# Performance work log

Measured on AMD Instinct MI355X. Metric: run time of the kernel, lower is better.

The kernel has to match this reference:

```python
import jax, jax.numpy as jnp
import numpy as np

B, S, D, F = 8, 2048, 1024, 3072
EPS = 1e-6


def _rmsnorm(x, w):
    rms = jax.lax.rsqrt(jnp.mean(x * x, axis=-1, keepdims=True) + EPS)
    return x * rms * w


def _scan_causal(x_scan, a):
    # h_t = a_t * h_{t-1} + x_t, over time axis. x_scan, a: [B,S,D]
    def step(h, inp):
        xs, at = inp
        h = at * h + xs
        return h, h
    xs_t = jnp.swapaxes(x_scan, 0, 1)  # [S,B,D]
    a_t = jnp.swapaxes(a, 0, 1)
    h0 = jnp.zeros(x_scan.shape[::2], dtype=x_scan.dtype)  # [B,D]
    _, out = jax.lax.scan(step, h0, (xs_t, a_t))
    return jnp.swapaxes(out, 0, 1)  # [B,S,D]


def setup_inputs() -> dict:
    key = jax.random.key(0)
    ks = jax.random.split(key, 12)
    sd = 1.0 / np.sqrt(D)
    sf = 1.0 / np.sqrt(F)
    return {
        "x": jax.random.normal(ks[0], (B, S, D), dtype=jnp.float32),
        "rms_mix_w": jnp.ones((D,), jnp.float32),
        "rms_ffn_w": jnp.ones((D,), jnp.float32),
        "Wg": jax.random.uniform(ks[1], (D, D), jnp.float32, -sd, sd),
        "bg": jax.random.uniform(ks[2], (D,), jnp.float32, -sd, sd),
        "Wv": jax.random.uniform(ks[3], (D, D), jnp.float32, -sd, sd),
        "bv": jax.random.uniform(ks[4], (D,), jnp.float32, -sd, sd),
        "Wd": jax.random.uniform(ks[5], (D, D), jnp.float32, -sd, sd),
        "bd": jnp.full((D,), 1.0, jnp.float32),  # decay_bias_init = 1.0
        "W_gate": jax.random.uniform(ks[6], (F, D), jnp.float32, -sd, sd),
        "W_up": jax.random.uniform(ks[7], (F, D), jnp.float32, -sd, sd),
        "W_out": jax.random.uniform(ks[8], (D, F), jnp.float32, -sf, sf),
    }


def reference(x, rms_mix_w, rms_ffn_w, Wg, bg, Wv, bv, Wd, bd, W_gate, W_up, W_out):
    # --- MinGRU mixer with pre-RMSNorm and residual ---
    xn = _rmsnorm(x, rms_mix_w)
    g = jnp.einsum("bsd,ed->bse", xn, Wg) + bg
    v = jnp.einsum("bsd,ed->bse", xn, Wv) + bv
    d = jnp.einsum("bsd,ed->bse", xn, Wd) + bd
    x_scan = jax.nn.sigmoid(g) * jnp.tanh(v)
    a = 0.001 + 0.998 * jax.nn.sigmoid(d)
    x = x + _scan_causal(x_scan, a)
    # --- SwiGLU FFN with pre-RMSNorm and residual ---
    xn = _rmsnorm(x, rms_ffn_w)
    gate = jax.nn.silu(jnp.einsum("bsd,fd->bsf", xn, W_gate))
    up = jnp.einsum("bsd,fd->bsf", xn, W_up)
    x = x + jnp.einsum("bsf,df->bsd", gate * up, W_out)
    return x
```

## Files before the change

### kernel.cpp

```cpp
#include <hip/hip_runtime.h>
#include <cstdint>
#include <cstddef>

typedef unsigned short u16;
typedef __attribute__((ext_vector_type(4))) float f32x4;
typedef __attribute__((ext_vector_type(8))) short s16x8;

#define BB 8
#define SS 2048
#define DD 1024
#define FF 3072
#define MM (BB*SS)
#define NCH 64
#define LCH (SS/NCH)

__device__ __forceinline__ float bf2f(u16 u){ union{uint32_t i;float f;}v; v.i=((uint32_t)u)<<16; return v.f; }
__device__ __forceinline__ u16 f2bf(float f){ union{float f;uint32_t i;}v; v.f=f; uint32_t r=v.i+0x7FFFu+((v.i>>16)&1u); return (u16)(r>>16); }
__device__ __forceinline__ float sigm(float x){ return 1.f/(1.f+__expf(-x)); }
__device__ __forceinline__ float tanh_f(float x){ return 2.f*sigm(2.f*x)-1.f; }

__global__ void conv_all(const float* __restrict__ Wg, const float* __restrict__ Wv,
                         const float* __restrict__ Wd, const float* __restrict__ Wgate,
                         const float* __restrict__ Wup, const float* __restrict__ Wout,
                         const float* __restrict__ rfw,
                         u16* __restrict__ oGvd, u16* __restrict__ oGu, u16* __restrict__ oWo){
  const int blk = blockIdx.x;
  if (blk < 3072) {
    size_t i = ((size_t)blk*256 + threadIdx.x)*4;
    int row = (int)(i >> 10); int col = (int)(i & 1023);
    const float* src; int srow;
    if (row < 2048) { int grp = row >> 5, w = row & 31; src = (w < 16) ? Wg : Wv; srow = grp*16 + (w & 15); }
    else            { src = Wd; srow = row - 2048; }
    float4 v = *(const float4*)(src + (size_t)srow*1024 + col);
    ushort4 o; o.x=f2bf(v.x); o.y=f2bf(v.y); o.z=f2bf(v.z); o.w=f2bf(v.w);
    *(ushort4*)(oGvd + i) = o;
  } else if (blk < 9216) {
    size_t i = ((size_t)(blk-3072)*256 + threadIdx.x)*4;
    int row = (int)(i >> 10); int col = (int)(i & 1023);
    int group = row >> 5, w = row & 31;
    const float* src = (w < 16) ? Wgate : Wup;
    int srow = group*16 + (w & 15);
    float4 v = *(const float4*)(src + (size_t)srow*1024 + col);
    float4 s = *(const float4*)(rfw + col);
    ushort4 o; o.x=f2bf(v.x*s.x); o.y=f2bf(v.y*s.y); o.z=f2bf(v.z*s.z); o.w=f2bf(v.w*s.w);
    *(ushort4*)(oGu + i) = o;
  } else {
    size_t i = ((size_t)(blk-9216)*256 + threadIdx.x)*4;
    float4 v = *(const float4*)(Wout + i);
    ushort4 o; o.x=f2bf(v.x); o.y=f2bf(v.y); o.z=f2bf(v.z); o.w=f2bf(v.w);
    *(ushort4*)(oWo + i) = o;
  }
}

__global__ void rmsnorm_k(const float* __restrict__ x, const float* __restrict__ wgt,
                          u16* __restrict__ out){
  const int row = blockIdx.x, t = threadIdx.x;
  float4 v = ((const float4*)(x + (size_t)row*DD))[t];
  float ss = v.x*v.x + v.y*v.y + v.z*v.z + v.w*v.w;
  #pragma unroll
  for (int o = 32; o > 0; o >>= 1) ss += __shfl_down(ss, o, 64);
  __shared__ float sacc[4];
  if ((t & 63) == 0) sacc[t >> 6] = ss;
  __syncthreads();
  float tot = sacc[0] + sacc[1] + sacc[2] + sacc[3];
  float r = rsqrtf(tot * (1.f/(float)DD) + 1e-6f);
  float4 wv = ((const float4*)wgt)[t];
  ushort4 o; o.x=f2bf(v.x*r*wv.x); o.y=f2bf(v.y*r*wv.y); o.z=f2bf(v.z*r*wv.z); o.w=f2bf(v.w*r*wv.w);
  ((ushort4*)(out + (size_t)row*DD))[t] = o;
}

template<int EPI, int NTN>
__global__ __launch_bounds__(512) void gemm256(
    const u16* __restrict__ A, const u16* __restrict__ Bm, int K,
    const float* __restrict__ bg, const float* __restrict__ bv, const float* __restrict__ bd,
    const float* __restrict__ rinv,
    u16* __restrict__ o_xs, u16* __restrict__ o_a,
    u16* __restrict__ o_h, const u16* __restrict__ yres, float* __restrict__ o_out)
{
  __shared__ u16 lds[2*32768];
  const int tid = threadIdx.x, w = tid >> 6, l = tid & 63;
  const int wr = w >> 2, wc = w & 3;
  const int nwg = gridDim.x, bid = blockIdx.x;
  const int sw = (bid & 7) * (nwg >> 3) + (bid >> 3);
  const int tm = sw / NTN, tn = sw % NTN;

  const int srow  = w*8 + (l >> 3);
  const int sslot = (l & 7) ^ ((l >> 3) & 7);
  const u16* gA = A  + (size_t)(tm*256 + srow)*K + sslot*8;
  const u16* gB = Bm + (size_t)(tn*256 + srow)*K + sslot*8;

#define STAGE_HALF(dbuf, isB, h, tile) do { \
    const u16* gsrc_ = ((isB) ? gB : gA) + ((size_t)(h)*128)*K + (size_t)(tile)*64; \
    u16* ldst_ = &lds[(dbuf)*32768 + (isB)*16384 + (h)*8192 + w*512]; \
    __builtin_amdgcn_global_load_lds((const __attribute__((address_space(1))) void*)gsrc_, \
        (__attribute__((address_space(3))) void*)ldst_, 16, 0, 0); \
    __builtin_amdgcn_global_load_lds((const __attribute__((address_space(1))) void*)(gsrc_ + (size_t)64*K), \
        (__attribute__((address_space(3))) void*)(ldst_ + 4096), 16, 0, 0); \
  } while(0)

  const int aRow = wr*128 + (l & 15);
  const int bRow = wc*64  + (l & 15);
  const int sl0  = (((l >> 4) ^ (l & 7))) * 8;

#define LDA(cb, mi, ks) (*(const s16x8*)&lds[(cb)*32768 + (aRow + (mi)*16)*64 + (sl0 ^ ((ks)*32))])
#define LDB(cb, ni, ks) (*(const s16x8*)&lds[(cb)*32768 + 16384 + (bRow + (ni)*16)*64 + (sl0 ^ ((ks)*32))])

#define LOADB(cb) do { \
    bfr[0][0]=LDB(cb,0,0); bfr[0][1]=LDB(cb,0,1); \
    bfr[1][0]=LDB(cb,1,0); bfr[1][1]=LDB(cb,1,1); \
    bfr[2][0]=LDB(cb,2,0); bfr[2][1]=LDB(cb,2,1); \
    bfr[3][0]=LDB(cb,3,0); bfr[3][1]=LDB(cb,3,1); \
  } while(0)

#define PHASE(cb, mi0, STAGE_STMT, ...) do { \
    s16x8 a00 = LDA(cb, (mi0),   0), a01 = LDA(cb, (mi0),   1); \
    s16x8 a10 = LDA(cb, (mi0)+1, 0), a11 = LDA(cb, (mi0)+1, 1); \
    STAGE_STMT; \
    __builtin_amdgcn_s_barrier(); \
    asm volatile("s_waitcnt lgkmcnt(0)" ::: "memory"); \
    __builtin_amdgcn_s_setprio(1); \
    acc[(mi0)  ][0] = __builtin_amdgcn_mfma_f32_16x16x32_bf16(a00, bfr[0][0], acc[(mi0)  ][0],0,0,0); \
    acc[(mi0)  ][1] = __builtin_amdgcn_mfma_f32_16x16x32_bf16(a00, bfr[1][0], acc[(mi0)  ][1],0,0,0); \
    acc[(mi0)  ][2] = __builtin_amdgcn_mfma_f32_16x16x32_bf16(a00, bfr[2][0], acc[(mi0)  ][2],0,0,0); \
    acc[(mi0)  ][3] = __builtin_amdgcn_mfma_f32_16x16x32_bf16(a00, bfr[3][0], acc[(mi0)  ][3],0,0,0); \
    acc[(mi0)+1][0] = __builtin_amdgcn_mfma_f32_16x16x32_bf16(a10, bfr[0][0], acc[(mi0)+1][0],0,0,0); \
    acc[(mi0)+1][1] = __builtin_amdgcn_mfma_f32_16x16x32_bf16(a10, bfr[1][0], acc[(mi0)+1][1],0,0,0); \
    acc[(mi0)+1][2] = __builtin_amdgcn_mfma_f32_16x16x32_bf16(a10, bfr[2][0], acc[(mi0)+1][2],0,0,0); \
    acc[(mi0)+1][3] = __builtin_amdgcn_mfma_f32_16x16x32_bf16(a10, bfr[3][0], acc[(mi0)+1][3],0,0,0); \
    acc[(mi0)  ][0] = __builtin_amdgcn_mfma_f32_16x16x32_bf16(a01, bfr[0][1], acc[(mi0)  ][0],0,0,0); \
    acc[(mi0)  ][1] = __builtin_amdgcn_mfma_f32_16x16x32_bf16(a01, bfr[1][1], acc[(mi0)  ][1],0,0,0); \
    acc[(mi0)  ][2] = __builtin_amdgcn_mfma_f32_16x16x32_bf16(a01, bfr[2][1], acc[(mi0)  ][2],0,0,0); \
    acc[(mi0)  ][3] = __builtin_amdgcn_mfma_f32_16x16x32_bf16(a01, bfr[3][1], acc[(mi0)  ][3],0,0,0); \
    acc[(mi0)+1][0] = __builtin_amdgcn_mfma_f32_16x16x32_bf16(a11, bfr[0][1], acc[(mi0)+1][0],0,0,0); \
    acc[(mi0)+1][1] = __builtin_amdgcn_mfma_f32_16x16x32_bf16(a11, bfr[1][1], acc[(mi0)+1][1],0,0,0); \
    acc[(mi0)+1][2] = __builtin_amdgcn_mfma_f32_16x16x32_bf16(a11, bfr[2][1], acc[(mi0)+1][2],0,0,0); \
    acc[(mi0)+1][3] = __builtin_amdgcn_mfma_f32_16x16x32_bf16(a11, bfr[3][1], acc[(mi0)+1][3],0,0,0); \
    __builtin_amdgcn_s_setprio(0); \
    __VA_ARGS__; \
    __builtin_amdgcn_s_barrier(); \
  } while(0)

  f32x4 acc[8][4] = {};
  s16x8 bfr[4][2];
  const int nk = K >> 6;

  STAGE_HALF(0,0,0,0); STAGE_HALF(0,0,1,0);
  STAGE_HALF(0,1,0,0); STAGE_HALF(0,1,1,0);
  STAGE_HALF(1,1,0,1); STAGE_HALF(1,1,1,1);
  asm volatile("s_waitcnt vmcnt(4)" ::: "memory");
  __builtin_amdgcn_s_barrier();

  for (int it = 0, t = 0; it < (nk >> 1); ++it, t += 2) {
    const int tp1 = t + 1;
    int tp2 = t + 2; if (tp2 >= nk) tp2 -= nk;
    int tp3 = t + 3; if (tp3 >= nk) tp3 -= nk;
    LOADB(0);
    PHASE(0, 0, STAGE_HALF(1,0,0,tp1), );
    PHASE(0, 2, STAGE_HALF(1,0,1,tp1), );
    PHASE(0, 4, STAGE_HALF(0,1,0,tp2), );
    PHASE(0, 6, STAGE_HALF(0,1,1,tp2), asm volatile("s_waitcnt vmcnt(4)" ::: "memory"));
    LOADB(1);
    PHASE(1, 0, STAGE_HALF(0,0,0,tp2), );
    PHASE(1, 2, STAGE_HALF(0,0,1,tp2), );
    PHASE(1, 4, STAGE_HALF(1,1,0,tp3), );
    PHASE(1, 6, STAGE_HALF(1,1,1,tp3), asm volatile("s_waitcnt vmcnt(4)" ::: "memory"));
  }
#undef PHASE
#undef LOADB
#undef LDA
#undef LDB
#undef STAGE_HALF

  const int rb = tm*256 + wr*128 + ((l >> 4) << 2);
  const int lc = l & 15;
  if constexpr (EPI == 0) {
    if (tn < 8) {
      #pragma unroll
      for (int mi = 0; mi < 8; ++mi)
        #pragma unroll
        for (int j = 0; j < 2; ++j) {
          int f = tn*128 + wc*32 + j*16 + lc;
          float bgf = bg[f], bvf = bv[f];
          #pragma unroll
          for (int i = 0; i < 4; ++i) {
            int r = rb + mi*16 + i;
            float g2 = acc[mi][2*j][i]   + bgf;
            float v2 = acc[mi][2*j+1][i] + bvf;
            o_xs[(size_t)r*DD + f] = f2bf(sigm(g2) * tanh_f(v2));
          }
        }
    } else {
      #pragma unroll
      for (int mi = 0; mi < 8; ++mi)
        #pragma unroll
        for (int ni = 0; ni < 4; ++ni) {
          int c = (tn-8)*256 + wc*64 + ni*16 + lc;
          float bdc = bd[c];
          #pragma unroll
          for (int i = 0; i < 4; ++i) {
            int r = rb + mi*16 + i;
            o_a[(size_t)r*DD + c] = f2bf(0.001f + 0.998f*sigm(acc[mi][ni][i] + bdc));
          }
        }
    }
  } else if constexpr (EPI == 1) {
    #pragma unroll
    for (int mi = 0; mi < 8; ++mi) {
      float4 rv = *(const float4*)&rinv[rb + mi*16];
      #pragma unroll
      for (int j = 0; j < 2; ++j) {
        int f = tn*128 + wc*32 + j*16 + lc;
        #pragma unroll
        for (int i = 0; i < 4; ++i) {
          int r = rb + mi*16 + i;
          float rvi = (i==0) ? rv.x : (i==1) ? rv.y : (i==2) ? rv.z : rv.w;
          float g2 = acc[mi][2*j][i]*rvi, u2 = acc[mi][2*j+1][i]*rvi;
          o_h[(size_t)r*FF + f] = f2bf(g2 * sigm(g2) * u2);
        }
      }
    }
  } else {
    #pragma unroll
    for (int mi = 0; mi < 8; ++mi)
      #pragma unroll
      for (int ni = 0; ni < 4; ++ni) {
        int c = tn*256 + wc*64 + ni*16 + lc;
        #pragma unroll
        for (int i = 0; i < 4; ++i) {
          int r = rb + mi*16 + i;
          size_t idx = (size_t)r*DD + c;
          o_out[idx] = bf2f(yres[idx]) + acc[mi][ni][i];
        }
      }
  }
}

__global__ void scan_pass1(const u16* __restrict__ xs, const u16* __restrict__ ab,
                           float* __restrict__ Ac, float* __restrict__ Xc){
  const int bid = blockIdx.x;
  const int d = ((bid & 3) << 8) + threadIdx.x;
  const int c = (bid >> 2) & (NCH-1);
  const int b = bid >> 8;
  size_t base = ((size_t)b*SS + (size_t)c*LCH)*DD + d;
  float A = 1.f, X = 0.f;
  for (int tt = 0; tt < LCH; ++tt){
    size_t idx = base + (size_t)tt*DD;
    float a = bf2f(ab[idx]);
    X = a*X + bf2f(xs[idx]); A *= a;
  }
  size_t o = ((size_t)b*NCH + c)*DD + d;
  Ac[o] = A; Xc[o] = X;
}

__global__ void scan_pass2(const float* __restrict__ Ac, const float* __restrict__ Xc,
                           float* __restrict__ hin){
  int gid = blockIdx.x*256 + threadIdx.x;
  int b = gid >> 10, d = gid & 1023;
  float h = 0.f;
  for (int c = 0; c < NCH; ++c){
    size_t o = ((size_t)b*NCH + c)*DD + d;
    hin[o] = h;
    h = Ac[o]*h + Xc[o];
  }
}

__global__ __launch_bounds__(256) void scan_pass3_y(
    const u16* __restrict__ xs, const u16* __restrict__ ab,
    const float* __restrict__ hin, const float* __restrict__ x,
    u16* __restrict__ ybf, float* __restrict__ rinv)
{
  const int bid = blockIdx.x;
  const int c = bid & (NCH-1);
  const int b = bid >> 6;
  const int t = threadIdx.x;
  float h[4];
  size_t hb = ((size_t)b*NCH + c)*DD + t;
  #pragma unroll
  for (int j = 0; j < 4; ++j) h[j] = hin[hb + j*256];
  __shared__ float sred[4];
  size_t base = ((size_t)b*SS + (size_t)c*LCH)*DD + t;
  const int row0 = b*SS + c*LCH;
  for (int tt = 0; tt < LCH; ++tt){
    size_t rowb = base + (size_t)tt*DD;
    float yv[4]; float ss = 0.f;
    #pragma unroll
    for (int j = 0; j < 4; ++j){
      size_t idx = rowb + (size_t)j*256;
      float a = bf2f(ab[idx]);
      h[j] = a*h[j] + bf2f(xs[idx]);
      yv[j] = x[idx] + h[j];
      ss += yv[j]*yv[j];
    }
    #pragma unroll
    for (int o = 32; o > 0; o >>= 1) ss += __shfl_down(ss, o, 64);
    if ((t & 63) == 0) sred[t >> 6] = ss;
    __syncthreads();
    float tot = sred[0] + sred[1] + sred[2] + sred[3];
    float r = rsqrtf(tot * (1.f/(float)DD) + 1e-6f);
    if (t == 0) rinv[row0 + tt] = r;
    #pragma unroll
    for (int j = 0; j < 4; ++j){
      size_t idx = rowb + (size_t)j*256;
      ybf[idx] = f2bf(yv[j]);
    }
    __syncthreads();
  }
}

extern "C" void kernel_launch(void* const* d_in, const int* in_sizes, int n_in,
                              void* d_out, int out_size, void* d_ws, size_t ws_size,
                              hipStream_t stream) {
  const float* x     = (const float*)d_in[0];
  const float* rmw   = (const float*)d_in[1];
  const float* rfw   = (const float*)d_in[2];
  const float* Wg    = (const float*)d_in[3];
  const float* bg    = (const float*)d_in[4];
  const float* Wv    = (const float*)d_in[5];
  const float* bv    = (const float*)d_in[6];
  const float* Wd    = (const float*)d_in[7];
  const float* bd    = (const float*)d_in[8];
  const float* Wgate = (const float*)d_in[9];
  const float* Wup   = (const float*)d_in[10];
  const float* Wout  = (const float*)d_in[11];
  float* out = (float*)d_out;

  char* p = (char*)d_ws;
  u16*  xn    = (u16*)p;              p += (size_t)MM*DD*2;
  u16*  Wgvd  = (u16*)p;              p += (size_t)3072*1024*2;
  u16*  Wgu   = (u16*)p;              p += (size_t)6144*1024*2;
  u16*  Wo    = (u16*)p;              p += (size_t)1024*3072*2;
  char* big   = p;                    p += (size_t)MM*FF*2;
  u16*  xs    = (u16*)big;
  u16*  ab    = (u16*)(big + (size_t)MM*DD*2);
  u16*  hbuf  = (u16*)big;
  float* Ac   = (float*)p;            p += (size_t)BB*NCH*DD*4;
  float* Xc   = (float*)p;            p += (size_t)BB*NCH*DD*4;
  float* hin  = (float*)p;            p += (size_t)BB*NCH*DD*4;
  float* rinv = (float*)p;            p += (size_t)MM*4;
  u16*  ybf   = xn;

  conv_all<<<12288, 256, 0, stream>>>(Wg, Wv, Wd, Wgate, Wup, Wout, rfw, Wgvd, Wgu, Wo);

  rmsnorm_k<<<MM, 256, 0, stream>>>(x, rmw, xn);
  gemm256<0,12><<<64*12, 512, 0, stream>>>(xn, Wgvd, 1024,
      bg, bv, bd, nullptr, xs, ab, nullptr, nullptr, nullptr);
  scan_pass1<<<BB*NCH*4, 256, 0, stream>>>(xs, ab, Ac, Xc);
  scan_pass2<<<32, 256, 0, stream>>>(Ac, Xc, hin);
  scan_pass3_y<<<BB*NCH, 256, 0, stream>>>(xs, ab, hin, x, ybf, rinv);

  gemm256<1,24><<<64*24, 512, 0, stream>>>(ybf, Wgu, 1024,
      nullptr, nullptr, nullptr, rinv, nullptr, nullptr, hbuf, nullptr, nullptr);
  gemm256<2,4><<<64*4, 512, 0, stream>>>(hbuf, Wo, 3072,
      nullptr, nullptr, nullptr, nullptr, nullptr, nullptr, nullptr, ybf, out);
}
```

Measured before the change: 511.4 us.

## Make GEMM blocks persistent over several N tiles with cross-tile prefetch

Each GEMM workgroup now computes T consecutive 256-wide N tiles for the same M tile instead of one. The grid shrinks to 256 or 512 blocks, so each one fits a single wave on the CUs. The k-loop prefetch wraps into the next tile's B panel so the pipeline stays primed across tiles. The goal is to cut tail-wave imbalance and launch/prologue overhead. The cost is that the epilogue now runs serialized inside each block, which can stall the MFMA pipeline between tiles.

```diff
diff --git a/kernel.cpp b/kernel.cpp
--- a/kernel.cpp
+++ b/kernel.cpp
@@ -69,7 +69,7 @@
   ((ushort4*)(out + (size_t)row*DD))[t] = o;
 }
 
-template<int EPI, int NTN>
+template<int EPI, int NTN, int T>
 __global__ __launch_bounds__(512) void gemm256(
     const u16* __restrict__ A, const u16* __restrict__ Bm, int K,
     const float* __restrict__ bg, const float* __restrict__ bv, const float* __restrict__ bd,
@@ -80,18 +80,28 @@
   __shared__ u16 lds[2*32768];
   const int tid = threadIdx.x, w = tid >> 6, l = tid & 63;
   const int wr = w >> 2, wc = w & 3;
+  constexpr int NBN = NTN / T;
   const int nwg = gridDim.x, bid = blockIdx.x;
   const int sw = (bid & 7) * (nwg >> 3) + (bid >> 3);
-  const int tm = sw / NTN, tn = sw % NTN;
+  const int tm = sw / NBN, tn0 = (sw % NBN) * T;
 
   const int srow  = w*8 + (l >> 3);
   const int sslot = (l & 7) ^ ((l >> 3) & 7);
-  const u16* gA = A  + (size_t)(tm*256 + srow)*K + sslot*8;
-  const u16* gB = Bm + (size_t)(tn*256 + srow)*K + sslot*8;
-
-#define STAGE_HALF(dbuf, isB, h, tile) do { \
-    const u16* gsrc_ = ((isB) ? gB : gA) + ((size_t)(h)*128)*K + (size_t)(tile)*64; \
-    u16* ldst_ = &lds[(dbuf)*32768 + (isB)*16384 + (h)*8192 + w*512]; \
+  const u16* gA  = A  + (size_t)(tm*256  + srow)*K + sslot*8;
+  const u16* gBc = Bm + (size_t)(tn0*256 + srow)*K + sslot*8;
+
+#define STAGE_A(dbuf, h, kt) do { \
+    const u16* gsrc_ = gA + ((size_t)(h)*128)*K + (size_t)(kt)*64; \
+    u16* ldst_ = &lds[(dbuf)*32768 + (h)*8192 + w*512]; \
+    __builtin_amdgcn_global_load_lds((const __attribute__((address_space(1))) void*)gsrc_, \
+        (__attribute__((address_space(3))) void*)ldst_, 16, 0, 0); \
+    __builtin_amdgcn_global_load_lds((const __attribute__((address_space(1))) void*)(gsrc_ + (size_t)64*K), \
+        (__attribute__((address_space(3))) void*)(ldst_ + 4096), 16, 0, 0); \
+  } while(0)
+
+#define STAGE_B(dbuf, h, bp, kt) do { \
+    const u16* gsrc_ = (bp) + ((size_t)(h)*128)*K + (size_t)(kt)*64; \
+    u16* ldst_ = &lds[(dbuf)*32768 + 16384 + (h)*8192 + w*512]; \
     __builtin_amdgcn_global_load_lds((const __attribute__((address_space(1))) void*)gsrc_, \
         (__attribute__((address_space(3))) void*)ldst_, 16, 0, 0); \
     __builtin_amdgcn_global_load_lds((const __attribute__((address_space(1))) void*)(gsrc_ + (size_t)64*K), \
@@ -144,95 +154,111 @@
   s16x8 bfr[4][2];
   const int nk = K >> 6;
 
-  STAGE_HALF(0,0,0,0); STAGE_HALF(0,0,1,0);
-  STAGE_HALF(0,1,0,0); STAGE_HALF(0,1,1,0);
-  STAGE_HALF(1,1,0,1); STAGE_HALF(1,1,1,1);
+  STAGE_A(0,0,0); STAGE_A(0,1,0);
+  STAGE_B(0,0,gBc,0); STAGE_B(0,1,gBc,0);
+  STAGE_B(1,0,gBc,1); STAGE_B(1,1,gBc,1);
   asm volatile("s_waitcnt vmcnt(4)" ::: "memory");
   __builtin_amdgcn_s_barrier();
 
-  for (int it = 0, t = 0; it < (nk >> 1); ++it, t += 2) {
-    const int tp1 = t + 1;
-    int tp2 = t + 2; if (tp2 >= nk) tp2 -= nk;
-    int tp3 = t + 3; if (tp3 >= nk) tp3 -= nk;
-    LOADB(0);
-    PHASE(0, 0, STAGE_HALF(1,0,0,tp1), );
-    PHASE(0, 2, STAGE_HALF(1,0,1,tp1), );
-    PHASE(0, 4, STAGE_HALF(0,1,0,tp2), );
-    PHASE(0, 6, STAGE_HALF(0,1,1,tp2), asm volatile("s_waitcnt vmcnt(4)" ::: "memory"));
-    LOADB(1);
-    PHASE(1, 0, STAGE_HALF(0,0,0,tp2), );
-    PHASE(1, 2, STAGE_HALF(0,0,1,tp2), );
-    PHASE(1, 4, STAGE_HALF(1,1,0,tp3), );
-    PHASE(1, 6, STAGE_HALF(1,1,1,tp3), asm volatile("s_waitcnt vmcnt(4)" ::: "memory"));
-  }
-#undef PHASE
-#undef LOADB
-#undef LDA
-#undef LDB
-#undef STAGE_HALF
-
-  const int rb = tm*256 + wr*128 + ((l >> 4) << 2);
-  const int lc = l & 15;
-  if constexpr (EPI == 0) {
-    if (tn < 8) {
+  #pragma unroll 1
+  for (int tile = 0; tile < T; ++tile) {
+    const u16* gBn = (tile + 1 < T) ? (gBc + (size_t)256*K) : gBc;
+    #pragma unroll 1
+    for (int it = 0, t = 0; it < (nk >> 1); ++it, t += 2) {
+      const int tp1 = t + 1;
+      int kt2 = t + 2; const u16* gB2 = gBc;
+      if (kt2 >= nk) { kt2 -= nk; gB2 = gBn; }
+      int kt3 = t + 3; const u16* gB3 = gBc;
+      if (kt3 >= nk) { kt3 -= nk; gB3 = gBn; }
+      LOADB(0);
+      PHASE(0, 0, STAGE_A(1,0,tp1), );
+      PHASE(0, 2, STAGE_A(1,1,tp1), );
+      PHASE(0, 4, STAGE_B(0,0,gB2,kt2), );
+      PHASE(0, 6, STAGE_B(0,1,gB2,kt2), asm volatile("s_waitcnt vmcnt(4)" ::: "memory"));
+      LOADB(1);
+      PHASE(1, 0, STAGE_A(0,0,kt2), );
+      PHASE(1, 2, STAGE_A(0,1,kt2), );
+      PHASE(1, 4, STAGE_B(1,0,gB3,kt3), );
+      PHASE(1, 6, STAGE_B(1,1,gB3,kt3), asm volatile("s_waitcnt vmcnt(4)" ::: "memory"));
+    }
+
+    const int tn = tn0 + tile;
+    const int rb = tm*256 + wr*128 + ((l >> 4) << 2);
+    const int lc = l & 15;
+    if constexpr (EPI == 0) {
+      if (tn < 8) {
+        #pragma unroll
+        for (int mi = 0; mi < 8; ++mi)
+          #pragma unroll
+          for (int j = 0; j < 2; ++j) {
+            int f = tn*128 + wc*32 + j*16 + lc;
+            float bgf = bg[f], bvf = bv[f];
+            #pragma unroll
+            for (int i = 0; i < 4; ++i) {
+              int r = rb + mi*16 + i;
+              float g2 = acc[mi][2*j][i]   + bgf;
+              float v2 = acc[mi][2*j+1][i] + bvf;
+              o_xs[(size_t)r*DD + f] = f2bf(sigm(g2) * tanh_f(v2));
+            }
+          }
+      } else {
+        #pragma unroll
+        for (int mi = 0; mi < 8; ++mi)
+          #pragma unroll
+          for (int ni = 0; ni < 4; ++ni) {
+            int c = (tn-8)*256 + wc*64 + ni*16 + lc;
+            float bdc = bd[c];
+            #pragma unroll
+            for (int i = 0; i < 4; ++i) {
+              int r = rb + mi*16 + i;
+              o_a[(size_t)r*DD + c] = f2bf(0.001f + 0.998f*sigm(acc[mi][ni][i] + bdc));
+            }
+          }
+      }
+    } else if constexpr (EPI == 1) {
       #pragma unroll
-      for (int mi = 0; mi < 8; ++mi)
+      for (int mi = 0; mi < 8; ++mi) {
+        float4 rv = *(const float4*)&rinv[rb + mi*16];
         #pragma unroll
         for (int j = 0; j < 2; ++j) {
           int f = tn*128 + wc*32 + j*16 + lc;
-          float bgf = bg[f], bvf = bv[f];
           #pragma unroll
           for (int i = 0; i < 4; ++i) {
             int r = rb + mi*16 + i;
-            float g2 = acc[mi][2*j][i]   + bgf;
-            float v2 = acc[mi][2*j+1][i] + bvf;
-            o_xs[(size_t)r*DD + f] = f2bf(sigm(g2) * tanh_f(v2));
+            float rvi = (i==0) ? rv.x : (i==1) ? rv.y : (i==2) ? rv.z : rv.w;
+            float g2 = acc[mi][2*j][i]*rvi, u2 = acc[mi][2*j+1][i]*rvi;
+            o_h[(size_t)r*FF + f] = f2bf(g2 * sigm(g2) * u2);
           }
         }
+      }
     } else {
       #pragma unroll
       for (int mi = 0; mi < 8; ++mi)
         #pragma unroll
         for (int ni = 0; ni < 4; ++ni) {
-          int c = (tn-8)*256 + wc*64 + ni*16 + lc;
-          float bdc = bd[c];
+          int c = tn*256 + wc*64 + ni*16 + lc;
           #pragma unroll
           for (int i = 0; i < 4; ++i) {
             int r = rb + mi*16 + i;
-            o_a[(size_t)r*DD + c] = f2bf(0.001f + 0.998f*sigm(acc[mi][ni][i] + bdc));
+            size_t idx = (size_t)r*DD + c;
+            o_out[idx] = bf2f(yres[idx]) + acc[mi][ni][i];
           }
         }
     }
-  } else if constexpr (EPI == 1) {
-    #pragma unroll
-    for (int mi = 0; mi < 8; ++mi) {
-      float4 rv = *(const float4*)&rinv[rb + mi*16];
-      #pragma unroll
-      for (int j = 0; j < 2; ++j) {
-        int f = tn*128 + wc*32 + j*16 + lc;
-        #pragma unroll
-        for (int i = 0; i < 4; ++i) {
-          int r = rb + mi*16 + i;
-          float rvi = (i==0) ? rv.x : (i==1) ? rv.y : (i==2) ? rv.z : rv.w;
-          float g2 = acc[mi][2*j][i]*rvi, u2 = acc[mi][2*j+1][i]*rvi;
-          o_h[(size_t)r*FF + f] = f2bf(g2 * sigm(g2) * u2);
-        }
-      }
-    }
-  } else {
+
     #pragma unroll
     for (int mi = 0; mi < 8; ++mi)
       #pragma unroll
-      for (int ni = 0; ni < 4; ++ni) {
-        int c = tn*256 + wc*64 + ni*16 + lc;
-        #pragma unroll
-        for (int i = 0; i < 4; ++i) {
-          int r = rb + mi*16 + i;
-          size_t idx = (size_t)r*DD + c;
-          o_out[idx] = bf2f(yres[idx]) + acc[mi][ni][i];
-        }
-      }
-  }
+      for (int ni = 0; ni < 4; ++ni)
+        acc[mi][ni] = (f32x4){0.f, 0.f, 0.f, 0.f};
+    gBc = gBn;
+  }
+#undef PHASE
+#undef LOADB
+#undef LDA
+#undef LDB
+#undef STAGE_A
+#undef STAGE_B
 }
 
 __global__ void scan_pass1(const u16* __restrict__ xs, const u16* __restrict__ ab,
@@ -342,14 +368,14 @@
   conv_all<<<12288, 256, 0, stream>>>(Wg, Wv, Wd, Wgate, Wup, Wout, rfw, Wgvd, Wgu, Wo);
 
   rmsnorm_k<<<MM, 256, 0, stream>>>(x, rmw, xn);
-  gemm256<0,12><<<64*12, 512, 0, stream>>>(xn, Wgvd, 1024,
+  gemm256<0,12,3><<<64*4, 512, 0, stream>>>(xn, Wgvd, 1024,
       bg, bv, bd, nullptr, xs, ab, nullptr, nullptr, nullptr);
   scan_pass1<<<BB*NCH*4, 256, 0, stream>>>(xs, ab, Ac, Xc);
   scan_pass2<<<32, 256, 0, stream>>>(Ac, Xc, hin);
   scan_pass3_y<<<BB*NCH, 256, 0, stream>>>(xs, ab, hin, x, ybf, rinv);
 
-  gemm256<1,24><<<64*24, 512, 0, stream>>>(ybf, Wgu, 1024,
+  gemm256<1,24,3><<<64*8, 512, 0, stream>>>(ybf, Wgu, 1024,
       nullptr, nullptr, nullptr, rinv, nullptr, nullptr, hbuf, nullptr, nullptr);
-  gemm256<2,4><<<64*4, 512, 0, stream>>>(hbuf, Wo, 3072,
+  gemm256<2,4,1><<<64*4, 512, 0, stream>>>(hbuf, Wo, 3072,
       nullptr, nullptr, nullptr, nullptr, nullptr, nullptr, nullptr, ybf, out);
 }
```

Measured after the change: 587.4 us. 14.9% more time.
